# Optimization experiments

Hardware: AMD Instinct MI355X
Metric: run time of the kernel (lower is better)

The kernel has to match this reference:

```python
import jax, jax.numpy as jnp
import numpy as np

TEMP = 0.5
EPS = 1e-12  # matches torch F.normalize default eps


def _l2_normalize(x):
    n = jnp.sqrt(jnp.sum(x * x, axis=1, keepdims=True))
    return x / jnp.maximum(n, EPS)


def setup_inputs() -> dict:
    key = jax.random.key(0)
    k1, k2 = jax.random.split(key)
    B, D = 4096, 256
    return {
        "x_i": jax.random.normal(k1, (B, D), dtype=jnp.float32),
        "x_j": jax.random.normal(k2, (B, D), dtype=jnp.float32),
    }


def reference(x_i, x_j):
    B = x_i.shape[0]
    z = jnp.concatenate([_l2_normalize(x_i), _l2_normalize(x_j)], axis=0)  # [2B, D]
    # cosine similarity of normalized vectors == plain matmul
    sim = z @ z.T  # [2B, 2B]
    pos = jnp.concatenate([jnp.diagonal(sim, B), jnp.diagonal(sim, -B)], axis=0)  # [2B]
    neg_mask = 1.0 - jnp.eye(2 * B, dtype=sim.dtype)
    denom = jnp.sum(neg_mask * jnp.exp(sim / TEMP), axis=1)  # [2B]
    # -log(exp(pos/T) / denom) = -pos/T + log(denom)
    loss = jnp.sum(-(pos / TEMP) + jnp.log(denom)) / (2 * B)
    return loss
```

## Files before the change

### kernel.cpp

```cpp
#include <hip/hip_runtime.h>
#include <hip/hip_bf16.h>

#define B_ROWS 4096
#define NROWS  8192
#define D      256
#define NSEG   48
#define NBLK2  768
#define TT     264

typedef __attribute__((ext_vector_type(4))) float floatx4;

__global__ __launch_bounds__(256) void norm_pos_kernel(
    const float* __restrict__ xi, const float* __restrict__ xj,
    unsigned char* __restrict__ z, float* __restrict__ pos,
    float* __restrict__ rowsum, float* __restrict__ out,
    unsigned int* __restrict__ counter) {
    int gt = blockIdx.x * 256 + threadIdx.x;
    if (gt < NROWS) rowsum[gt] = 0.f;
    if (gt == 0) { out[0] = 0.f; counter[0] = 0u; }

    int p    = blockIdx.x * 4 + (threadIdx.x >> 6);
    int lane = threadIdx.x & 63;
    float4 v1 = ((const float4*)(xi + (size_t)p * D))[lane];
    float4 v2 = ((const float4*)(xj + (size_t)p * D))[lane];
    float ss1 = v1.x * v1.x + v1.y * v1.y + v1.z * v1.z + v1.w * v1.w;
    float ss2 = v2.x * v2.x + v2.y * v2.y + v2.z * v2.z + v2.w * v2.w;
#pragma unroll
    for (int off = 32; off > 0; off >>= 1) {
        ss1 += __shfl_xor(ss1, off);
        ss2 += __shfl_xor(ss2, off);
    }
    float sc1 = 1.0f / fmaxf(sqrtf(ss1), 1e-12f);
    float sc2 = 1.0f / fmaxf(sqrtf(ss2), 1e-12f);

    float n1x = v1.x * sc1, n1y = v1.y * sc1, n1z = v1.z * sc1, n1w = v1.w * sc1;
    float n2x = v2.x * sc2, n2y = v2.y * sc2, n2z = v2.z * sc2, n2w = v2.w * sc2;

    float dp = n1x * n2x + n1y * n2y + n1z * n2z + n1w * n2w;
#pragma unroll
    for (int off = 32; off > 0; off >>= 1) dp += __shfl_xor(dp, off);
    if (lane == 0) { pos[p] = dp; pos[p + B_ROWS] = dp; }

    int q1 = __builtin_amdgcn_cvt_pk_fp8_f32(n1x, n1y, 0, false);
    q1     = __builtin_amdgcn_cvt_pk_fp8_f32(n1z, n1w, q1, true);
    int q2 = __builtin_amdgcn_cvt_pk_fp8_f32(n2x, n2y, 0, false);
    q2     = __builtin_amdgcn_cvt_pk_fp8_f32(n2z, n2w, q2, true);
    ((int*)(z + (size_t)p * D))[lane]            = q1;
    ((int*)(z + (size_t)(p + B_ROWS) * D))[lane] = q2;
}

__global__ __launch_bounds__(256, 3) void sim_rowsum_kernel(
    const unsigned char* __restrict__ z, float* __restrict__ rowsum,
    const float* __restrict__ pos, unsigned int* __restrict__ counter,
    float* __restrict__ out) {
    __shared__ __align__(16) int4 Bbuf[2][512];
    __shared__ unsigned int done_s;
    __shared__ float sdata[4];

    const int tid  = threadIdx.x;
    const int lane = tid & 63;
    const int w    = tid >> 6;
    const int lm   = lane & 15;
    const int lg   = lane >> 4;

    const int s  = blockIdx.x / NSEG;
    const int q  = blockIdx.x % NSEG;
    const int L0 = 256 - 8 * s;
    const int cb = (q * TT) / NSEG;
    const int ce = ((q + 1) * TT) / NSEG;

    const int scol = tid & 31;
    const int ssg  = tid >> 5;

    const int crow = lg >> 1;
    const int half = (lg & 1) * 8;

    long long a[8][4];
    floatx4 acc[4][2];
    float rsacc[4][4];
    int4 pf0, pf1;

#pragma unroll
    for (int mi = 0; mi < 4; mi++)
#pragma unroll
        for (int r = 0; r < 4; r++) rsacc[mi][r] = 0.f;

    auto decode = [&](int c, int& panel, int& colbase, int& cloc) {
        if (c < L0) { panel = s;      cloc = c; }
        else        { panel = 31 - s; cloc = c - L0; }
        colbase = panel * 256 + cloc * 32;
    };

    auto loadA = [&](int panel) {
#pragma unroll
        for (int kk = 0; kk < 8; kk++)
#pragma unroll
            for (int mi = 0; mi < 4; mi++)
                a[kk][mi] = *(const long long*)(
                    z + (size_t)(panel * 256 + w * 64 + mi * 16 + lm) * D +
                    kk * 32 + lg * 8);
    };

    auto flushRs = [&](int panel) {
#pragma unroll
        for (int mi = 0; mi < 4; mi++)
#pragma unroll
            for (int r = 0; r < 4; r++) {
                float v = rsacc[mi][r];
                v += __shfl_xor(v, 1); v += __shfl_xor(v, 2);
                v += __shfl_xor(v, 4); v += __shfl_xor(v, 8);
                if (lm == 0)
                    atomicAdd(&rowsum[panel * 256 + w * 64 + mi * 16 + lg * 4 + r], v);
                rsacc[mi][r] = 0.f;
            }
    };

    auto fetch = [&](int colbase) {
        const unsigned char* p = z + (size_t)(colbase + scol) * D + ssg * 32;
        pf0 = *(const int4*)p;
        pf1 = *(const int4*)(p + 16);
    };
    auto writeB = [&](int buf) {
        Bbuf[buf][(ssg * 2 + 0) * 32 + scol] = pf0;
        Bbuf[buf][(ssg * 2 + 1) * 32 + scol] = pf1;
    };

    int panel, colbase, cloc;
    decode(cb, panel, colbase, cloc);
    int curpanel = panel;
    fetch(colbase);
    writeB(0);
    loadA(panel);
    __syncthreads();

    for (int c = cb; c < ce; c++) {
        const int buf = (c - cb) & 1;
        decode(c, panel, colbase, cloc);

        const bool hn = (c + 1 < ce);
        if (hn) {
            int npanel, ncolbase, ncloc;
            decode(c + 1, npanel, ncolbase, ncloc);
            fetch(ncolbase);
        }
        if (panel != curpanel) {
            flushRs(curpanel);
            loadA(panel);
            curpanel = panel;
        }

#pragma unroll
        for (int mi = 0; mi < 4; mi++)
#pragma unroll
            for (int ni = 0; ni < 2; ni++)
                acc[mi][ni] = (floatx4){0.f, 0.f, 0.f, 0.f};

        const char* bbase = (const char*)Bbuf[buf];
#pragma unroll
        for (int kk = 0; kk < 8; kk++) {
            long long b0 = *(const long long*)(
                bbase + (((kk * 2 + crow) * 32 + lm) * 16) + half);
            long long b1 = *(const long long*)(
                bbase + (((kk * 2 + crow) * 32 + 16 + lm) * 16) + half);
#pragma unroll
            for (int mi = 0; mi < 4; mi++)
                acc[mi][0] = __builtin_amdgcn_mfma_f32_16x16x32_fp8_fp8(
                    a[kk][mi], b0, acc[mi][0], 0, 0, 0);
#pragma unroll
            for (int mi = 0; mi < 4; mi++)
                acc[mi][1] = __builtin_amdgcn_mfma_f32_16x16x32_fp8_fp8(
                    a[kk][mi], b1, acc[mi][1], 0, 0, 0);
        }

        const bool diagreg = (cloc < 8);
        float cs0 = 0.f, cs1 = 0.f;
        if (diagreg) {
            const int rowb = panel * 256 + w * 64 + lg * 4;
            const int col0 = colbase + lm, col1 = colbase + 16 + lm;
#pragma unroll
            for (int mi = 0; mi < 4; mi++)
#pragma unroll
                for (int r = 0; r < 4; r++) {
                    int grow = rowb + mi * 16 + r;
                    float e0 = (grow == col0) ? 0.f : __expf(2.0f * acc[mi][0][r]);
                    float e1 = (grow == col1) ? 0.f : __expf(2.0f * acc[mi][1][r]);
                    rsacc[mi][r] += e0 + e1;
                }
        } else {
#pragma unroll
            for (int mi = 0; mi < 4; mi++)
#pragma unroll
                for (int r = 0; r < 4; r++) {
                    float e0 = __expf(2.0f * acc[mi][0][r]);
                    float e1 = __expf(2.0f * acc[mi][1][r]);
                    rsacc[mi][r] += e0 + e1;
                    cs0 += e0; cs1 += e1;
                }
            cs0 += __shfl_xor(cs0, 16); cs0 += __shfl_xor(cs0, 32);
            cs1 += __shfl_xor(cs1, 16); cs1 += __shfl_xor(cs1, 32);
            if (lane < 16) {
                atomicAdd(&rowsum[colbase + lane],      cs0);
                atomicAdd(&rowsum[colbase + 16 + lane], cs1);
            }
        }

        if (hn) {
            writeB(buf ^ 1);
            __syncthreads();
        }
    }
    flushRs(curpanel);

    __syncthreads();
    if (tid == 0) {
        __threadfence();
        done_s = atomicAdd(counter, 1u);
    }
    __syncthreads();
    if (done_s == (unsigned int)(NBLK2 - 1)) {
        __threadfence();
        float acc_l = 0.f;
#pragma unroll 4
        for (int r = tid; r < NROWS; r += 256) {
            float rsv = __hip_atomic_load(&rowsum[r], __ATOMIC_RELAXED,
                                          __HIP_MEMORY_SCOPE_AGENT);
            acc_l += -2.0f * pos[r] + logf(rsv);
        }
#pragma unroll
        for (int off = 32; off > 0; off >>= 1) acc_l += __shfl_xor(acc_l, off);
        if (lane == 0) sdata[w] = acc_l;
        __syncthreads();
        if (tid == 0)
            out[0] = (sdata[0] + sdata[1] + sdata[2] + sdata[3]) / (float)NROWS;
    }
}

extern "C" void kernel_launch(void* const* d_in, const int* in_sizes, int n_in,
                              void* d_out, int out_size, void* d_ws, size_t ws_size,
                              hipStream_t stream) {
    const float* xi = (const float*)d_in[0];
    const float* xj = (const float*)d_in[1];
    float* out      = (float*)d_out;

    char* ws        = (char*)d_ws;
    unsigned char* z = (unsigned char*)ws;
    float* rowsum   = (float*)(ws + (size_t)NROWS * D);
    float* pos      = rowsum + NROWS;
    unsigned int* counter = (unsigned int*)(pos + NROWS);

    norm_pos_kernel<<<B_ROWS / 4, 256, 0, stream>>>(xi, xj, z, pos,
                                                    rowsum, out, counter);
    sim_rowsum_kernel<<<NBLK2, 256, 0, stream>>>(z, rowsum, pos, counter, out);
}
```

Measured before the change: 109.7 us.

## Retile symmetric sim kernel to 128-row strips with 64-column tiles

Changes the upper-triangle tiling from 256-row panels with 32-column tiles to 128-row strips with 64-column tiles, and raises the block count and occupancy hint to 4 blocks per CU. Each wave now holds 2x16 rows of A in registers instead of 4x16, loads four B fragments per k-step, and issues atomics on 64 columns per tile. The aim is better work balance and more resident waves, at the price of more A reloads and more rowsum atomics per element.

```diff
diff --git a/kernel.cpp b/kernel.cpp
--- a/kernel.cpp
+++ b/kernel.cpp
@@ -4,9 +4,9 @@
 #define B_ROWS 4096
 #define NROWS  8192
 #define D      256
-#define NSEG   48
-#define NBLK2  768
-#define TT     264
+#define NSEG   32
+#define NBLK2  1024
+#define TPP    130
 
 typedef __attribute__((ext_vector_type(4))) float floatx4;
 
@@ -49,11 +49,11 @@
     ((int*)(z + (size_t)(p + B_ROWS) * D))[lane] = q2;
 }
 
-__global__ __launch_bounds__(256, 3) void sim_rowsum_kernel(
+__global__ __launch_bounds__(256, 4) void sim_rowsum_kernel(
     const unsigned char* __restrict__ z, float* __restrict__ rowsum,
     const float* __restrict__ pos, unsigned int* __restrict__ counter,
     float* __restrict__ out) {
-    __shared__ __align__(16) int4 Bbuf[2][512];
+    __shared__ __align__(16) int4 Bbuf[2][1024];
     __shared__ unsigned int done_s;
     __shared__ float sdata[4];
 
@@ -63,144 +63,147 @@
     const int lm   = lane & 15;
     const int lg   = lane >> 4;
 
-    const int s  = blockIdx.x / NSEG;
-    const int q  = blockIdx.x % NSEG;
-    const int L0 = 256 - 8 * s;
-    const int cb = (q * TT) / NSEG;
-    const int ce = ((q + 1) * TT) / NSEG;
-
-    const int scol = tid & 31;
-    const int ssg  = tid >> 5;
-
-    const int crow = lg >> 1;
-    const int half = (lg & 1) * 8;
-
-    long long a[8][4];
-    floatx4 acc[4][2];
-    float rsacc[4][4];
-    int4 pf0, pf1;
-
-#pragma unroll
-    for (int mi = 0; mi < 4; mi++)
+    const int s  = blockIdx.x >> 5;
+    const int q  = blockIdx.x & 31;
+    const int L0 = 128 - 2 * s;
+    const int cb = (q * TPP) >> 5;
+    const int ce = ((q + 1) * TPP) >> 5;
+
+    const int scol  = tid >> 2;
+    const int spart = tid & 3;
+
+    long long a[8][2];
+    floatx4 acc[2][4];
+    float rsacc[2][4];
+    int4 pf[4];
+
+#pragma unroll
+    for (int mi = 0; mi < 2; mi++)
 #pragma unroll
         for (int r = 0; r < 4; r++) rsacc[mi][r] = 0.f;
 
-    auto decode = [&](int c, int& panel, int& colbase, int& cloc) {
-        if (c < L0) { panel = s;      cloc = c; }
-        else        { panel = 31 - s; cloc = c - L0; }
-        colbase = panel * 256 + cloc * 32;
-    };
-
-    auto loadA = [&](int panel) {
+    auto decode = [&](int c, int& strip, int& colbase, int& cloc) {
+        if (c < L0) { strip = s;      cloc = c; }
+        else        { strip = 63 - s; cloc = c - L0; }
+        colbase = strip * 128 + cloc * 64;
+    };
+
+    auto loadA = [&](int strip) {
 #pragma unroll
         for (int kk = 0; kk < 8; kk++)
 #pragma unroll
-            for (int mi = 0; mi < 4; mi++)
+            for (int mi = 0; mi < 2; mi++)
                 a[kk][mi] = *(const long long*)(
-                    z + (size_t)(panel * 256 + w * 64 + mi * 16 + lm) * D +
+                    z + (size_t)(strip * 128 + w * 32 + mi * 16 + lm) * D +
                     kk * 32 + lg * 8);
     };
 
-    auto flushRs = [&](int panel) {
-#pragma unroll
-        for (int mi = 0; mi < 4; mi++)
+    auto flushRs = [&](int strip) {
+#pragma unroll
+        for (int mi = 0; mi < 2; mi++)
 #pragma unroll
             for (int r = 0; r < 4; r++) {
                 float v = rsacc[mi][r];
                 v += __shfl_xor(v, 1); v += __shfl_xor(v, 2);
                 v += __shfl_xor(v, 4); v += __shfl_xor(v, 8);
                 if (lm == 0)
-                    atomicAdd(&rowsum[panel * 256 + w * 64 + mi * 16 + lg * 4 + r], v);
+                    atomicAdd(&rowsum[strip * 128 + w * 32 + mi * 16 + lg * 4 + r], v);
                 rsacc[mi][r] = 0.f;
             }
     };
 
     auto fetch = [&](int colbase) {
-        const unsigned char* p = z + (size_t)(colbase + scol) * D + ssg * 32;
-        pf0 = *(const int4*)p;
-        pf1 = *(const int4*)(p + 16);
+        const unsigned char* p = z + (size_t)(colbase + scol) * D + spart * 16;
+#pragma unroll
+        for (int j = 0; j < 4; j++) pf[j] = *(const int4*)(p + j * 64);
     };
     auto writeB = [&](int buf) {
-        Bbuf[buf][(ssg * 2 + 0) * 32 + scol] = pf0;
-        Bbuf[buf][(ssg * 2 + 1) * 32 + scol] = pf1;
-    };
-
-    int panel, colbase, cloc;
-    decode(cb, panel, colbase, cloc);
-    int curpanel = panel;
+#pragma unroll
+        for (int j = 0; j < 4; j++)
+            Bbuf[buf][(spart + 4 * j) * 64 + scol] = pf[j];
+    };
+
+    int strip, colbase, cloc;
+    decode(cb, strip, colbase, cloc);
+    int curstrip = strip;
     fetch(colbase);
     writeB(0);
-    loadA(panel);
+    loadA(strip);
     __syncthreads();
 
     for (int c = cb; c < ce; c++) {
         const int buf = (c - cb) & 1;
-        decode(c, panel, colbase, cloc);
+        decode(c, strip, colbase, cloc);
 
         const bool hn = (c + 1 < ce);
         if (hn) {
-            int npanel, ncolbase, ncloc;
-            decode(c + 1, npanel, ncolbase, ncloc);
-            fetch(ncolbase);
-        }
-        if (panel != curpanel) {
-            flushRs(curpanel);
-            loadA(panel);
-            curpanel = panel;
-        }
-
-#pragma unroll
-        for (int mi = 0; mi < 4; mi++)
-#pragma unroll
-            for (int ni = 0; ni < 2; ni++)
+            int ns, ncb, ncl;
+            decode(c + 1, ns, ncb, ncl);
+            fetch(ncb);
+        }
+        if (strip != curstrip) {
+            flushRs(curstrip);
+            loadA(strip);
+            curstrip = strip;
+        }
+
+#pragma unroll
+        for (int mi = 0; mi < 2; mi++)
+#pragma unroll
+            for (int ni = 0; ni < 4; ni++)
                 acc[mi][ni] = (floatx4){0.f, 0.f, 0.f, 0.f};
 
         const char* bbase = (const char*)Bbuf[buf];
 #pragma unroll
         for (int kk = 0; kk < 8; kk++) {
-            long long b0 = *(const long long*)(
-                bbase + (((kk * 2 + crow) * 32 + lm) * 16) + half);
-            long long b1 = *(const long long*)(
-                bbase + (((kk * 2 + crow) * 32 + 16 + lm) * 16) + half);
-#pragma unroll
-            for (int mi = 0; mi < 4; mi++)
-                acc[mi][0] = __builtin_amdgcn_mfma_f32_16x16x32_fp8_fp8(
-                    a[kk][mi], b0, acc[mi][0], 0, 0, 0);
-#pragma unroll
-            for (int mi = 0; mi < 4; mi++)
-                acc[mi][1] = __builtin_amdgcn_mfma_f32_16x16x32_fp8_fp8(
-                    a[kk][mi], b1, acc[mi][1], 0, 0, 0);
-        }
-
-        const bool diagreg = (cloc < 8);
-        float cs0 = 0.f, cs1 = 0.f;
+            long long b[4];
+#pragma unroll
+            for (int ni = 0; ni < 4; ni++)
+                b[ni] = *(const long long*)(
+                    bbase + (((kk * 2 + (lg >> 1)) * 64 + ni * 16 + lm) * 16) +
+                    (lg & 1) * 8);
+#pragma unroll
+            for (int mi = 0; mi < 2; mi++)
+#pragma unroll
+                for (int ni = 0; ni < 4; ni++)
+                    acc[mi][ni] = __builtin_amdgcn_mfma_f32_16x16x32_fp8_fp8(
+                        a[kk][mi], b[ni], acc[mi][ni], 0, 0, 0);
+        }
+
+        const bool diagreg = (cloc < 2);
+        float cs[4] = {0.f, 0.f, 0.f, 0.f};
         if (diagreg) {
-            const int rowb = panel * 256 + w * 64 + lg * 4;
-            const int col0 = colbase + lm, col1 = colbase + 16 + lm;
-#pragma unroll
-            for (int mi = 0; mi < 4; mi++)
-#pragma unroll
-                for (int r = 0; r < 4; r++) {
-                    int grow = rowb + mi * 16 + r;
-                    float e0 = (grow == col0) ? 0.f : __expf(2.0f * acc[mi][0][r]);
-                    float e1 = (grow == col1) ? 0.f : __expf(2.0f * acc[mi][1][r]);
-                    rsacc[mi][r] += e0 + e1;
+            const int rowb = strip * 128 + w * 32 + lg * 4;
+#pragma unroll
+            for (int mi = 0; mi < 2; mi++)
+#pragma unroll
+                for (int ni = 0; ni < 4; ni++) {
+                    const int gcol = colbase + ni * 16 + lm;
+#pragma unroll
+                    for (int r = 0; r < 4; r++) {
+                        int grow = rowb + mi * 16 + r;
+                        float e = (grow == gcol) ? 0.f
+                                                 : __expf(2.0f * acc[mi][ni][r]);
+                        rsacc[mi][r] += e;
+                    }
                 }
         } else {
 #pragma unroll
-            for (int mi = 0; mi < 4; mi++)
-#pragma unroll
-                for (int r = 0; r < 4; r++) {
-                    float e0 = __expf(2.0f * acc[mi][0][r]);
-                    float e1 = __expf(2.0f * acc[mi][1][r]);
-                    rsacc[mi][r] += e0 + e1;
-                    cs0 += e0; cs1 += e1;
-                }
-            cs0 += __shfl_xor(cs0, 16); cs0 += __shfl_xor(cs0, 32);
-            cs1 += __shfl_xor(cs1, 16); cs1 += __shfl_xor(cs1, 32);
-            if (lane < 16) {
-                atomicAdd(&rowsum[colbase + lane],      cs0);
-                atomicAdd(&rowsum[colbase + 16 + lane], cs1);
+            for (int mi = 0; mi < 2; mi++)
+#pragma unroll
+                for (int ni = 0; ni < 4; ni++)
+#pragma unroll
+                    for (int r = 0; r < 4; r++) {
+                        float e = __expf(2.0f * acc[mi][ni][r]);
+                        rsacc[mi][r] += e;
+                        cs[ni]      += e;
+                    }
+#pragma unroll
+            for (int ni = 0; ni < 4; ni++) {
+                float v = cs[ni];
+                v += __shfl_xor(v, 16); v += __shfl_xor(v, 32);
+                if (lane < 16)
+                    atomicAdd(&rowsum[colbase + ni * 16 + lane], v);
             }
         }
 
@@ -209,7 +212,7 @@
             __syncthreads();
         }
     }
-    flushRs(curpanel);
+    flushRs(curstrip);
 
     __syncthreads();
     if (tid == 0) {
```

After: 123.1 us. 12.2% more time.

## Make each wave own a 64-row strip with private swizzled LDS tile, no block barriers

Applied to the files above, without the earlier changes.

Work is now split per wave instead of per block. Each wave takes a 64-row strip paired with its mirror strip for the triangular schedule, and loads its own 32-column B tile into a private LDS slice with an XOR swizzle. This removes the block-wide __syncthreads and double buffering inside the main loop and balances work at a finer grain. In exchange, each wave fetches its own B tile, so global/L2 traffic rises and B data is no longer shared across the four waves. The single LDS buffer is overwritten after compute, relying on in-order wave execution.

```diff
diff --git a/kernel.cpp b/kernel.cpp
--- a/kernel.cpp
+++ b/kernel.cpp
@@ -5,8 +5,10 @@
 #define NROWS  8192
 #define D      256
 #define NSEG   48
-#define NBLK2  768
-#define TT     264
+#define SPAIRS 64
+#define NWAVES (SPAIRS * NSEG)
+#define NBLK2  (NWAVES / 4)
+#define TPW    258
 
 typedef __attribute__((ext_vector_type(4))) float floatx4;
 
@@ -53,7 +55,7 @@
     const unsigned char* __restrict__ z, float* __restrict__ rowsum,
     const float* __restrict__ pos, unsigned int* __restrict__ counter,
     float* __restrict__ out) {
-    __shared__ __align__(16) int4 Bbuf[2][512];
+    __shared__ __align__(16) char Bsl[4][8192];
     __shared__ unsigned int done_s;
     __shared__ float sdata[4];
 
@@ -63,45 +65,44 @@
     const int lm   = lane & 15;
     const int lg   = lane >> 4;
 
-    const int s  = blockIdx.x / NSEG;
-    const int q  = blockIdx.x % NSEG;
-    const int L0 = 256 - 8 * s;
-    const int cb = (q * TT) / NSEG;
-    const int ce = ((q + 1) * TT) / NSEG;
-
-    const int scol = tid & 31;
-    const int ssg  = tid >> 5;
-
-    const int crow = lg >> 1;
-    const int half = (lg & 1) * 8;
+    char* myB = Bsl[w];
+
+    const int wid = blockIdx.x * 4 + w;
+    const int s   = wid / NSEG;
+    const int q   = wid % NSEG;
+    const int L0  = 256 - 2 * s;
+    const int cb  = (q * TPW) / NSEG;
+    const int ce  = ((q + 1) * TPW) / NSEG;
+
+    const int fcol = lane >> 4;
+    const int fc16 = lane & 15;
 
     long long a[8][4];
     floatx4 acc[4][2];
     float rsacc[4][4];
-    int4 pf0, pf1;
+    int4 pf[8];
 
 #pragma unroll
     for (int mi = 0; mi < 4; mi++)
 #pragma unroll
         for (int r = 0; r < 4; r++) rsacc[mi][r] = 0.f;
 
-    auto decode = [&](int c, int& panel, int& colbase, int& cloc) {
-        if (c < L0) { panel = s;      cloc = c; }
-        else        { panel = 31 - s; cloc = c - L0; }
-        colbase = panel * 256 + cloc * 32;
-    };
-
-    auto loadA = [&](int panel) {
+    auto decode = [&](int c, int& strip, int& colbase, int& cloc) {
+        if (c < L0) { strip = s;       cloc = c; }
+        else        { strip = 127 - s; cloc = c - L0; }
+        colbase = strip * 64 + cloc * 32;
+    };
+
+    auto loadA = [&](int strip) {
 #pragma unroll
         for (int kk = 0; kk < 8; kk++)
 #pragma unroll
             for (int mi = 0; mi < 4; mi++)
                 a[kk][mi] = *(const long long*)(
-                    z + (size_t)(panel * 256 + w * 64 + mi * 16 + lm) * D +
-                    kk * 32 + lg * 8);
-    };
-
-    auto flushRs = [&](int panel) {
+                    z + (size_t)(strip * 64 + mi * 16 + lm) * D + kk * 32 + lg * 8);
+    };
+
+    auto flushRs = [&](int strip) {
 #pragma unroll
         for (int mi = 0; mi < 4; mi++)
 #pragma unroll
@@ -110,43 +111,46 @@
                 v += __shfl_xor(v, 1); v += __shfl_xor(v, 2);
                 v += __shfl_xor(v, 4); v += __shfl_xor(v, 8);
                 if (lm == 0)
-                    atomicAdd(&rowsum[panel * 256 + w * 64 + mi * 16 + lg * 4 + r], v);
+                    atomicAdd(&rowsum[strip * 64 + mi * 16 + lg * 4 + r], v);
                 rsacc[mi][r] = 0.f;
             }
     };
 
     auto fetch = [&](int colbase) {
-        const unsigned char* p = z + (size_t)(colbase + scol) * D + ssg * 32;
-        pf0 = *(const int4*)p;
-        pf1 = *(const int4*)(p + 16);
-    };
-    auto writeB = [&](int buf) {
-        Bbuf[buf][(ssg * 2 + 0) * 32 + scol] = pf0;
-        Bbuf[buf][(ssg * 2 + 1) * 32 + scol] = pf1;
-    };
-
-    int panel, colbase, cloc;
-    decode(cb, panel, colbase, cloc);
-    int curpanel = panel;
+        const unsigned char* p = z + (size_t)colbase * D + lane * 16;
+#pragma unroll
+        for (int j = 0; j < 8; j++)
+            pf[j] = *(const int4*)(p + j * 1024);
+    };
+    auto writeB = [&]() {
+#pragma unroll
+        for (int j = 0; j < 8; j++) {
+            const int col = 4 * j + fcol;
+            const int u   = fc16 * 32 + (col ^ (fc16 & 7));
+            *(int4*)(myB + u * 16) = pf[j];
+        }
+    };
+
+    int strip, colbase, cloc;
+    decode(cb, strip, colbase, cloc);
+    int curstrip = strip;
     fetch(colbase);
-    writeB(0);
-    loadA(panel);
-    __syncthreads();
+    writeB();
+    loadA(strip);
 
     for (int c = cb; c < ce; c++) {
-        const int buf = (c - cb) & 1;
-        decode(c, panel, colbase, cloc);
+        decode(c, strip, colbase, cloc);
 
         const bool hn = (c + 1 < ce);
         if (hn) {
-            int npanel, ncolbase, ncloc;
-            decode(c + 1, npanel, ncolbase, ncloc);
-            fetch(ncolbase);
-        }
-        if (panel != curpanel) {
-            flushRs(curpanel);
-            loadA(panel);
-            curpanel = panel;
+            int ns, ncb2, ncl;
+            decode(c + 1, ns, ncb2, ncl);
+            fetch(ncb2);
+        }
+        if (strip != curstrip) {
+            flushRs(curstrip);
+            loadA(strip);
+            curstrip = strip;
         }
 
 #pragma unroll
@@ -155,13 +159,15 @@
             for (int ni = 0; ni < 2; ni++)
                 acc[mi][ni] = (floatx4){0.f, 0.f, 0.f, 0.f};
 
-        const char* bbase = (const char*)Bbuf[buf];
+        const int half = (lg & 1) * 8;
 #pragma unroll
         for (int kk = 0; kk < 8; kk++) {
+            const int c16 = kk * 2 + (lg >> 1);
+            const int x   = c16 & 7;
             long long b0 = *(const long long*)(
-                bbase + (((kk * 2 + crow) * 32 + lm) * 16) + half);
+                myB + (c16 * 32 + ((0 * 16 + lm) ^ x)) * 16 + half);
             long long b1 = *(const long long*)(
-                bbase + (((kk * 2 + crow) * 32 + 16 + lm) * 16) + half);
+                myB + (c16 * 32 + ((1 * 16 + lm) ^ x)) * 16 + half);
 #pragma unroll
             for (int mi = 0; mi < 4; mi++)
                 acc[mi][0] = __builtin_amdgcn_mfma_f32_16x16x32_fp8_fp8(
@@ -172,21 +178,23 @@
                     a[kk][mi], b1, acc[mi][1], 0, 0, 0);
         }
 
-        const bool diagreg = (cloc < 8);
-        float cs0 = 0.f, cs1 = 0.f;
-        if (diagreg) {
-            const int rowb = panel * 256 + w * 64 + lg * 4;
-            const int col0 = colbase + lm, col1 = colbase + 16 + lm;
-#pragma unroll
-            for (int mi = 0; mi < 4; mi++)
-#pragma unroll
-                for (int r = 0; r < 4; r++) {
-                    int grow = rowb + mi * 16 + r;
-                    float e0 = (grow == col0) ? 0.f : __expf(2.0f * acc[mi][0][r]);
-                    float e1 = (grow == col1) ? 0.f : __expf(2.0f * acc[mi][1][r]);
-                    rsacc[mi][r] += e0 + e1;
+        if (cloc < 2) {
+            const int rowb = strip * 64 + lg * 4;
+#pragma unroll
+            for (int mi = 0; mi < 4; mi++)
+#pragma unroll
+                for (int ni = 0; ni < 2; ni++) {
+                    const int gcol = colbase + ni * 16 + lm;
+#pragma unroll
+                    for (int r = 0; r < 4; r++) {
+                        const int grow = rowb + mi * 16 + r;
+                        float e = (grow == gcol) ? 0.f
+                                                 : __expf(2.0f * acc[mi][ni][r]);
+                        rsacc[mi][r] += e;
+                    }
                 }
         } else {
+            float cs0 = 0.f, cs1 = 0.f;
 #pragma unroll
             for (int mi = 0; mi < 4; mi++)
 #pragma unroll
@@ -204,12 +212,9 @@
             }
         }
 
-        if (hn) {
-            writeB(buf ^ 1);
-            __syncthreads();
-        }
-    }
-    flushRs(curpanel);
+        if (hn) writeB();
+    }
+    flushRs(curstrip);
 
     __syncthreads();
     if (tid == 0) {
@@ -242,10 +247,10 @@
     const float* xj = (const float*)d_in[1];
     float* out      = (float*)d_out;
 
-    char* ws        = (char*)d_ws;
+    char* ws         = (char*)d_ws;
     unsigned char* z = (unsigned char*)ws;
-    float* rowsum   = (float*)(ws + (size_t)NROWS * D);
-    float* pos      = rowsum + NROWS;
+    float* rowsum    = (float*)(ws + (size_t)NROWS * D);
+    float* pos       = rowsum + NROWS;
     unsigned int* counter = (unsigned int*)(pos + NROWS);
 
     norm_pos_kernel<<<B_ROWS / 4, 256, 0, stream>>>(xi, xj, z, pos,
```

Result: slower. 142.7 us (+30.1%).
